# Kernel optimization log

Hardware: AMD Instinct MI355X
Metric: run time of the kernel (lower is better)

Reference implementation:

```python
import jax, jax.numpy as jnp
import numpy as np

H, C = 4, 64          # heads, per-head channels
NB, NG = 30000, 6000  # bus nodes, gen nodes
EL, EG = 250000, 12000

def setup_inputs():
    ks = iter(jax.random.split(jax.random.key(0), 64))
    def nrm(shape, scale=1.0):
        return jax.random.normal(next(ks), shape, jnp.float32) * scale
    inp = {}
    inp['x_bus'] = nrm((NB, 32))
    inp['x_gen'] = nrm((NG, 16))
    inp['ea_line'] = jax.random.uniform(next(ks), (EL, 6), jnp.float32)
    inp['ea_g2b'] = jax.random.uniform(next(ks), (EG, 6), jnp.float32)
    inp['ea_b2g'] = jax.random.uniform(next(ks), (EG, 6), jnp.float32)
    inp['proj_gen_w'] = nrm((16, 32), 16 ** -0.5)
    inp['proj_gen_b'] = jnp.zeros((32,), jnp.float32)
    for l, (din, dout) in enumerate([(32, 256), (256, 256), (256, 64)]):
        sc = din ** -0.5
        inp['Wl%d' % l] = nrm((3, din, H * C), sc)
        inp['Wr%d' % l] = nrm((3, din, H * C), sc)
        inp['We%d' % l] = nrm((3, 6, H * C), 6 ** -0.5)
        inp['att%d' % l] = nrm((3, H, C), 0.1)
        inp['bc%d' % l] = jnp.zeros((3, dout), jnp.float32)
        inp['temp%d' % l] = jnp.ones((3,), jnp.float32)
        inp['lnw%d' % l] = jnp.ones((2, dout), jnp.float32)
        inp['lnb%d' % l] = jnp.zeros((2, dout), jnp.float32)
    inp['rp0_w'] = nrm((2, 32, 256), 32 ** -0.5)
    inp['rp0_b'] = jnp.zeros((2, 256), jnp.float32)
    inp['rp2_w'] = nrm((2, 256, 64), 256 ** -0.5)
    inp['rp2_b'] = jnp.zeros((2, 64), jnp.float32)
    inp['src_line'] = jax.random.randint(next(ks), (EL,), 0, NB, jnp.int32)
    inp['dst_line'] = jax.random.randint(next(ks), (EL,), 0, NB, jnp.int32)
    inp['src_g2b'] = jax.random.randint(next(ks), (EG,), 0, NG, jnp.int32)
    inp['dst_g2b'] = jax.random.randint(next(ks), (EG,), 0, NB, jnp.int32)
    inp['src_b2g'] = jax.random.randint(next(ks), (EG,), 0, NB, jnp.int32)
    inp['dst_b2g'] = jax.random.randint(next(ks), (EG,), 0, NG, jnp.int32)
    return inp

def _conv(xs, xd, src, dst, ea, Wl, Wr, We, att, bias, temp, concat, nd):
    # PhysicsGATv2Conv: overwrite last edge-attr column with physics prior tau/|Z| (physics_weight=1, z_index=3)
    ea = ea.at[:, -1].set(temp / jnp.maximum(ea[:, 3], 1e-6))
    xl = (xs @ Wl).reshape(-1, H, C)   # [Ns,H,C]
    xr = (xd @ Wr).reshape(-1, H, C)   # [Nd,H,C]
    m = xl[src] + xr[dst] + (ea @ We).reshape(-1, H, C)  # [E,H,C]
    logits = (jax.nn.leaky_relu(m, 0.2) * att).sum(-1)   # [E,H]
    mx = jax.ops.segment_max(logits, dst, num_segments=nd)
    mx = jnp.where(jnp.isfinite(mx), mx, 0.0)
    ex = jnp.exp(logits - mx[dst])
    alpha = ex / (jax.ops.segment_sum(ex, dst, num_segments=nd)[dst] + 1e-16)
    o = jax.ops.segment_sum(xl[src] * alpha[..., None], dst, num_segments=nd)  # [Nd,H,C]
    o = o.reshape(nd, H * C) if concat else o.mean(1)
    return o + bias

def _ln(x, w, b):
    mu = x.mean(-1, keepdims=True)
    v = ((x - mu) ** 2).mean(-1, keepdims=True)
    return (x - mu) / jnp.sqrt(v + 1e-5) * w + b

def _fwd(x_bus, x_gen, ea_line, ea_g2b, ea_b2g, proj_gen_w, proj_gen_b,
         Wl0, Wr0, We0, att0, bc0, temp0, lnw0, lnb0,
         Wl1, Wr1, We1, att1, bc1, temp1, lnw1, lnb1,
         Wl2, Wr2, We2, att2, bc2, temp2, lnw2, lnb2,
         rp0_w, rp0_b, rp2_w, rp2_b,
         src_line, dst_line, src_g2b, dst_g2b, src_b2g, dst_b2g):
    xb = x_bus                               # bus projector is Identity (32 == max dim)
    xg = x_gen @ proj_gen_w + proj_gen_b     # gen 16 -> 32
    layers = [(Wl0, Wr0, We0, att0, bc0, temp0, lnw0, lnb0, True),
              (Wl1, Wr1, We1, att1, bc1, temp1, lnw1, lnb1, True),
              (Wl2, Wr2, We2, att2, bc2, temp2, lnw2, lnb2, False)]
    for l, (Wl, Wr, We, att, bc, tp, lw, lb, concat) in enumerate(layers):
        rb, rg = xb, xg
        # to_hetero aggr='sum': one conv per edge type, sum into destination node type
        ob = (_conv(xb, xb, src_line, dst_line, ea_line, Wl[0], Wr[0], We[0], att[0], bc[0], tp[0], concat, NB)
              + _conv(xg, xb, src_g2b, dst_g2b, ea_g2b, Wl[1], Wr[1], We[1], att[1], bc[1], tp[1], concat, NB))
        og = _conv(xb, xg, src_b2g, dst_b2g, ea_b2g, Wl[2], Wr[2], We[2], att[2], bc[2], tp[2], concat, NG)
        xb = _ln(ob, lw[0], lb[0])
        xg = _ln(og, lw[1], lb[1])
        if l == 0:
            xb = xb + rb @ rp0_w[0] + rp0_b[0]
            xg = xg + rg @ rp0_w[1] + rp0_b[1]
        elif l == 1:
            xb = xb + rb
            xg = xg + rg
        else:
            xb = xb + rb @ rp2_w[0] + rp2_b[0]
            xg = xg + rg @ rp2_w[1] + rp2_b[1]
        if l < 2:
            xb = jax.nn.elu(xb)
            xg = jax.nn.elu(xg)
    # output_projector is Identity (final_dim == output_dim == 64); concat node-type outputs
    return jnp.concatenate([xb, xg], 0)

def reference(x_bus, x_gen, ea_line, ea_g2b, ea_b2g, proj_gen_w, proj_gen_b,
              Wl0, Wr0, We0, att0, bc0, temp0, lnw0, lnb0,
              Wl1, Wr1, We1, att1, bc1, temp1, lnw1, lnb1,
              Wl2, Wr2, We2, att2, bc2, temp2, lnw2, lnb2,
              rp0_w, rp0_b, rp2_w, rp2_b,
              src_line, dst_line, src_g2b, dst_g2b, src_b2g, dst_b2g):
    return _fwd(x_bus, x_gen, ea_line, ea_g2b, ea_b2g, proj_gen_w, proj_gen_b,
                Wl0, Wr0, We0, att0, bc0, temp0, lnw0, lnb0,
                Wl1, Wr1, We1, att1, bc1, temp1, lnw1, lnb1,
                Wl2, Wr2, We2, att2, bc2, tem2 := temp2, lnw2, lnb2,
                rp0_w, rp0_b, rp2_w, rp2_b,
                src_line, dst_line, src_g2b, dst_g2b, src_b2g, dst_b2g)
```

## Files before the change

kernel.cpp:

```cpp
#include <hip/hip_runtime.h>
#include <math.h>

#define NBUS 30000
#define NGEN 6000
#define NEL 250000
#define NEG 12000

#define AS1 __attribute__((address_space(1)))
#define AS3 __attribute__((address_space(3)))

typedef unsigned short u16;
typedef __attribute__((ext_vector_type(8))) short bf16x8;
typedef __attribute__((ext_vector_type(4))) float f32x4;

__device__ __forceinline__ u16 f2b(float x) {
  unsigned u = __float_as_uint(x);
  unsigned r = (u + 0x7FFFu + ((u >> 16) & 1u)) >> 16;
  return (u16)r;
}
__device__ __forceinline__ float b2f(u16 x) {
  return __uint_as_float((unsigned)x << 16);
}
__device__ __forceinline__ f32x4 splat4(float v) {
  f32x4 r = {v, v, v, v};
  return r;
}
__device__ __forceinline__ f32x4 b2f4(ushort4 v) {
  f32x4 r;
  r.x = b2f(v.x); r.y = b2f(v.y); r.z = b2f(v.z); r.w = b2f(v.w);
  return r;
}

__global__ void zeroi(int* __restrict__ p, int n) {
  int i = blockIdx.x * blockDim.x + threadIdx.x;
  int st = gridDim.x * blockDim.x;
  for (; i < n; i += st) p[i] = 0;
}

__global__ void cast_k(const float* __restrict__ s, u16* __restrict__ d, int n) {
  int i = blockIdx.x * 256 + threadIdx.x;
  if (i < n) d[i] = f2b(s[i]);
}

struct CsrArgs {
  const int* dst[3];
  const int* src[3];
  const float* ea[3];
  const float* tmp0;
  const float* tmp1;
  const float* tmp2;
  int* cnt[3];
  int* rowptr[3];
  int* eidx[3];
  int* srcC[3];
  float* eaC[3];
  int* psum[3];
  int E[3];
  int N[3];
};

__global__ void hist_b(CsrArgs a) {
  int ty = blockIdx.y;
  int i = blockIdx.x * 256 + threadIdx.x;
  if (i < a.E[ty]) atomicAdd(&a.cnt[ty][a.dst[ty][i]], 1);
}

__global__ __launch_bounds__(1024) void scan_p1(CsrArgs a) {
  int ty = blockIdx.y;
  int n = a.N[ty];
  int base = blockIdx.x * 1024;
  if (base >= n) return;
  int tid = threadIdx.x, lane = tid & 63, wv = tid >> 6;
  int i = base + tid;
  int v = (i < n) ? a.cnt[ty][i] : 0;
#pragma unroll
  for (int off = 32; off >= 1; off >>= 1) v += __shfl_xor(v, off);
  __shared__ int w[16];
  if (lane == 0) w[wv] = v;
  __syncthreads();
  if (tid < 16) {
    int t = w[tid];
#pragma unroll
    for (int off = 8; off >= 1; off >>= 1) t += __shfl_xor(t, off, 16);
    if (tid == 0) a.psum[ty][blockIdx.x] = t;
  }
}

__global__ __launch_bounds__(64) void scan_p2(CsrArgs a) {
  int ty = blockIdx.y;
  int nb = (a.N[ty] + 1023) / 1024;
  int tid = threadIdx.x;
  int v = (tid < nb) ? a.psum[ty][tid] : 0;
  int x = v;
#pragma unroll
  for (int off = 1; off < 64; off <<= 1) {
    int y = __shfl_up(x, off, 64);
    if (tid >= off) x += y;
  }
  if (tid < nb) a.psum[ty][tid] = x - v;
}

__global__ __launch_bounds__(1024) void scan_p3(CsrArgs a) {
  int ty = blockIdx.y;
  int n = a.N[ty];
  int base = blockIdx.x * 1024;
  if (base >= n) return;
  int tid = threadIdx.x, lane = tid & 63, wv = tid >> 6;
  int i = base + tid;
  int v = (i < n) ? a.cnt[ty][i] : 0;
  int x = v;
#pragma unroll
  for (int off = 1; off < 64; off <<= 1) {
    int y = __shfl_up(x, off, 64);
    if (lane >= off) x += y;
  }
  __shared__ int w[16];
  if (lane == 63) w[wv] = x;
  __syncthreads();
  if (tid < 16) {
    int t = w[tid];
#pragma unroll
    for (int off = 1; off < 16; off <<= 1) {
      int y = __shfl_up(t, off, 16);
      if (tid >= off) t += y;
    }
    w[tid] = t;
  }
  __syncthreads();
  int woff = (wv == 0) ? 0 : w[wv - 1];
  int incl = a.psum[ty][blockIdx.x] + woff + x;
  if (i < n) {
    a.rowptr[ty][i + 1] = incl;
    a.cnt[ty][i] = incl - v;
  }
  if (i == 0) a.rowptr[ty][0] = 0;
}

__global__ void scatter_b(CsrArgs a) {
  int ty = blockIdx.y;
  int i = blockIdx.x * 256 + threadIdx.x;
  if (i < a.E[ty]) {
    int p = atomicAdd(&a.cnt[ty][a.dst[ty][i]], 1);
    a.eidx[ty][p] = i;
  }
}

__global__ void gather_b(CsrArgs a) {
  int ty = blockIdx.y;
  int i = blockIdx.x * 256 + threadIdx.x;
  if (i >= a.E[ty]) return;
  int e = a.eidx[ty][i];
  a.srcC[ty][i] = a.src[ty][e];
  const float* s = a.ea[ty] + (size_t)e * 6;
  float* d = a.eaC[ty] + (size_t)i * 8;
  float e3 = s[3];
  float inv = 1.f / fmaxf(e3, 1e-6f);
  d[0] = s[0]; d[1] = s[1]; d[2] = s[2]; d[3] = e3; d[4] = s[4];
  d[5] = a.tmp0[ty] * inv;
  d[6] = a.tmp1[ty] * inv;
  d[7] = a.tmp2[ty] * inv;
}

__global__ void gen_proj(const float* __restrict__ x, const float* __restrict__ w,
                         const float* __restrict__ b, u16* __restrict__ o16) {
  int idx = blockIdx.x * blockDim.x + threadIdx.x;
  if (idx >= NGEN * 32) return;
  int i = idx >> 5, c = idx & 31;
  float acc = b[c];
#pragma unroll
  for (int k = 0; k < 16; ++k) acc += x[i * 16 + k] * w[k * 32 + c];
  o16[idx] = f2b(acc);
}

struct PackArgs {
  const float* src[24];
  int off[24];
  int lgN[24];
  int total[24];
  int K[24];
};
__global__ void pack_multi(PackArgs a, u16* __restrict__ Wt) {
  int j = blockIdx.y;
  int idx = blockIdx.x * 256 + threadIdx.x;
  if (idx >= a.total[j]) return;
  int N1 = (1 << a.lgN[j]) - 1;
  int n = idx & N1;
  int k = idx >> a.lgN[j];
  Wt[(size_t)a.off[j] + (size_t)n * a.K[j] + k] = f2b(a.src[j][idx]);
}

__global__ __launch_bounds__(256) void gemm_both(
    const u16* __restrict__ Ab, const u16* __restrict__ Ag,
    const u16* __restrict__ Wt, int goff,
    u16* __restrict__ Cb, u16* __restrict__ Cg,
    int K, int Nb, int Ng, int ybus)
{
  __shared__ __align__(16) u16 As[128 * 32];
  __shared__ __align__(16) u16 Bs[128 * 32];
  const int t = threadIdx.x;
  const int w = t >> 6, lane = t & 63;
  const u16* A; const u16* W; u16* C; int M, Ncols, bn;
  if ((int)blockIdx.y < ybus) {
    A = Ab; W = Wt; C = Cb; M = NBUS; Ncols = Nb; bn = blockIdx.y * 128;
  } else {
    A = Ag; W = Wt + goff; C = Cg; M = NGEN; Ncols = Ng; bn = (blockIdx.y - ybus) * 128;
  }
  const int bm = blockIdx.x * 128;
  if (bm >= M) return;
  const int wm = (w & 1) * 64, wn = (w >> 1) * 64;
  const int lr = lane & 15, q = lane >> 4;
  const int srow = lane >> 2;
  const int blk = (lane & 3) ^ (srow & 3);
  f32x4 acc[4][4] = {};
  for (int k0 = 0; k0 < K; k0 += 32) {
#pragma unroll
    for (int sseg = 0; sseg < 2; ++sseg) {
      int seg = w + (sseg << 2);
      int row = (seg << 4) + srow;
      int ga = bm + row; if (ga > M - 1) ga = M - 1;
      const u16* gpa = A + (size_t)ga * K + k0 + (blk << 3);
      __builtin_amdgcn_global_load_lds((AS1 void*)gpa, (AS3 void*)(As + (seg << 9)),
                                       16, 0, 0);
      int gb = bn + row;
      const u16* gpb = W + (size_t)gb * K + k0 + (blk << 3);
      __builtin_amdgcn_global_load_lds((AS1 void*)gpb, (AS3 void*)(Bs + (seg << 9)),
                                       16, 0, 0);
    }
    __syncthreads();
    bf16x8 af[4], bg[4];
#pragma unroll
    for (int i = 0; i < 4; ++i) {
      int r = wm + i * 16 + lr;
      af[i] = *(const bf16x8*)&As[(r << 5) + ((q ^ (r & 3)) << 3)];
    }
#pragma unroll
    for (int j = 0; j < 4; ++j) {
      int r = wn + j * 16 + lr;
      bg[j] = *(const bf16x8*)&Bs[(r << 5) + ((q ^ (r & 3)) << 3)];
    }
#pragma unroll
    for (int i = 0; i < 4; ++i)
#pragma unroll
      for (int j = 0; j < 4; ++j)
        acc[i][j] = __builtin_amdgcn_mfma_f32_16x16x32_bf16(
            af[i], bg[j], acc[i][j], 0, 0, 0);
    __syncthreads();
  }
#pragma unroll
  for (int i = 0; i < 4; ++i) {
    int row0 = bm + wm + i * 16 + q * 4;
#pragma unroll
    for (int j = 0; j < 4; ++j) {
      int col = bn + wn + j * 16 + lr;
      if (col < Ncols) {
#pragma unroll
        for (int r = 0; r < 4; ++r) {
          int row = row0 + r;
          if (row < M) C[(size_t)row * Ncols + col] = f2b(acc[i][j][r]);
        }
      }
    }
  }
}


#define CS_F1(lv, ev, nv, tv, idx) do { \
    int rc_ = (idx) < nch ? (idx) : nch - 1; \
    lv = *(const ushort4*)(xl + (size_t)__builtin_amdgcn_readlane(vsrc, rc_) * ldl + ch); \
    const float* ep_ = eac + (size_t)(cb + rc_) * 8; \
    ev = *(const float4*)ep_; \
    nv = ep_[4]; \
    tv = ep_[4 + TS]; \
  } while (0)

#define CS_FETCH(S, base) do { \
    CS_F1(l##S##0, e##S##0, n##S##0, t##S##0, (base)); \
    CS_F1(l##S##1, e##S##1, n##S##1, t##S##1, (base) + 1); \
  } while (0)

#define CS_EDGE(xv, ev, nv, tv, pv) do { \
    f32x4 m_ = xv + rx; \
    m_ = __builtin_elementwise_fma(splat4(ev.x), w0, m_); \
    m_ = __builtin_elementwise_fma(splat4(ev.y), w1, m_); \
    m_ = __builtin_elementwise_fma(splat4(ev.z), w2, m_); \
    m_ = __builtin_elementwise_fma(splat4(ev.w), w3, m_); \
    m_ = __builtin_elementwise_fma(splat4(nv), w4, m_); \
    m_ = __builtin_elementwise_fma(splat4(tv), w5, m_); \
    m_ = __builtin_elementwise_max(m_, m_ * 0.2f); \
    pv = m_.x * av.x; \
    pv = fmaf(m_.y, av.y, pv); \
    pv = fmaf(m_.z, av.z, pv); \
    pv = fmaf(m_.w, av.w, pv); \
  } while (0)

#define CS_COMPUTE(S, base) do { \
    f32x4 x0_ = b2f4(l##S##0), x1_ = b2f4(l##S##1); \
    float p0_, p1_; \
    CS_EDGE(x0_, e##S##0, n##S##0, t##S##0, p0_); \
    CS_EDGE(x1_, e##S##1, n##S##1, t##S##1, p1_); \
    p0_ += __shfl_xor(p0_, 1); p0_ += __shfl_xor(p0_, 2); \
    p0_ += __shfl_xor(p0_, 4); p0_ += __shfl_xor(p0_, 8); \
    p1_ += __shfl_xor(p1_, 1); p1_ += __shfl_xor(p1_, 2); \
    p1_ += __shfl_xor(p1_, 4); p1_ += __shfl_xor(p1_, 8); \
    if ((base) >= nch) p0_ = -INFINITY; \
    if ((base) + 1 >= nch) p1_ = -INFINITY; \
    float nm_ = fmaxf(mx, fmaxf(p0_, p1_)); \
    float sc_ = __expf(mx - nm_); \
    float q0_ = __expf(p0_ - nm_), q1_ = __expf(p1_ - nm_); \
    mx = nm_; \
    den = den * sc_ + (q0_ + q1_); \
    acc = acc * splat4(sc_); \
    acc = __builtin_elementwise_fma(splat4(q0_), x0_, acc); \
    acc = __builtin_elementwise_fma(splat4(q1_), x1_, acc); \
  } while (0)

template<int TS>
__device__ __forceinline__ f32x4 conv_set(
    int node, int beg, int end, int ch,
    const int* __restrict__ srcc, const float* __restrict__ eac,
    const u16* __restrict__ xl, int ldl,
    const u16* __restrict__ xr, int ldr,
    const float* __restrict__ We, const float* __restrict__ att)
{
  f32x4 w0 = *(const f32x4*)(We + ch);
  f32x4 w1 = *(const f32x4*)(We + 256 + ch);
  f32x4 w2 = *(const f32x4*)(We + 512 + ch);
  f32x4 w3 = *(const f32x4*)(We + 768 + ch);
  f32x4 w4 = *(const f32x4*)(We + 1024 + ch);
  f32x4 w5 = *(const f32x4*)(We + 1280 + ch);
  f32x4 av = *(const f32x4*)(att + ch);
  f32x4 rx = b2f4(*(const ushort4*)(xr + (size_t)node * ldr + ch));
  float mx = -INFINITY, den = 0.f;
  f32x4 acc = {0.f, 0.f, 0.f, 0.f};
  int lane = ch >> 2;

  for (int cb = beg; cb < end; cb += 64) {
    int nch = end - cb;
    if (nch > 64) nch = 64;
    int li = lane < nch ? lane : nch - 1;
    int vsrc = srcc[cb + li];
    int np = (nch + 1) >> 1;

    ushort4 la0, la1, lb0, lb1;
    float4 ea0, ea1, eb0, eb1;
    float na0, na1, nb0, nb1;
    float ta0, ta1, tb0, tb1;

    CS_FETCH(a, 0);
    int g = 0;
    for (; g + 2 < np; g += 2) {
      CS_FETCH(b, (g + 1) << 1);
      CS_COMPUTE(a, g << 1);
      CS_FETCH(a, (g + 2) << 1);
      CS_COMPUTE(b, (g + 1) << 1);
    }
    if (g + 1 < np) {
      CS_FETCH(b, (g + 1) << 1);
      CS_COMPUTE(a, g << 1);
      CS_COMPUTE(b, (g + 1) << 1);
    } else {
      CS_COMPUTE(a, g << 1);
    }
  }
  float inv = 1.f / (den + 1e-16f);
  return acc * splat4(inv);
}

struct ConvP {
  const int* __restrict__ rpA; const int* __restrict__ srcA;
  const float* __restrict__ eaA;
  const u16* __restrict__ xlA; const u16* __restrict__ xrA;
  const float* __restrict__ WeA; const float* __restrict__ attA;
  const int* __restrict__ rpB; const int* __restrict__ srcB;
  const float* __restrict__ eaB;
  const u16* __restrict__ xlB; const u16* __restrict__ xrB;
  const float* __restrict__ WeB; const float* __restrict__ attB;
  const float* __restrict__ b1; const float* __restrict__ b2;
  const float* __restrict__ lnw; const float* __restrict__ lnb;
  const u16* __restrict__ res16;
  float* __restrict__ outf; u16* __restrict__ out16;
  int ldlA, ldrA, ldlB, ldrB, ld16, N;
};

template<int MODE, int TS>
__global__ __launch_bounds__(256) void conv_fused(ConvP bus, ConvP gen, int nbBus) {
  const bool isb = (int)blockIdx.x < nbBus;
  const int grp = isb ? blockIdx.x : blockIdx.x - nbBus;
#define SEL(f) (isb ? bus.f : gen.f)
  const int* __restrict__ rpA = SEL(rpA);
  const int* __restrict__ srcA = SEL(srcA);
  const float* __restrict__ eaA = SEL(eaA);
  const u16* __restrict__ xlA = SEL(xlA);
  const u16* __restrict__ xrA = SEL(xrA);
  const float* __restrict__ WeA = SEL(WeA);
  const float* __restrict__ attA = SEL(attA);
  const int* __restrict__ rpB = SEL(rpB);
  const int N = SEL(N);
  const int ldlA = SEL(ldlA), ldrA = SEL(ldrA);

  int node = grp * 4 + (threadIdx.x >> 6);
  int lane = threadIdx.x & 63;
  if (node >= N) return;
  int ch = lane << 2;
  int begA = rpA[node], endA = rpA[node + 1];
  int begB = 0, endB = 0;
  if (rpB) { begB = rpB[node]; endB = rpB[node + 1]; }
  f32x4 o = conv_set<TS>(node, begA, endA, ch, srcA, eaA, xlA, ldlA,
                         xrA, ldrA, WeA, attA);
  if (rpB && begB < endB) {
    f32x4 ob = conv_set<TS>(node, begB, endB, ch, SEL(srcB), SEL(eaB),
                            SEL(xlB), SEL(ldlB), SEL(xrB), SEL(ldrB),
                            SEL(WeB), SEL(attB));
    o[0] += ob[0]; o[1] += ob[1]; o[2] += ob[2]; o[3] += ob[3];
  }
  const float* __restrict__ b1 = SEL(b1);
  const float* __restrict__ b2 = SEL(b2);
  const float* __restrict__ lnw = SEL(lnw);
  const float* __restrict__ lnb = SEL(lnb);
  const u16* __restrict__ res16 = SEL(res16);
  const int ld16 = SEL(ld16);
  if (MODE == 0) {
    int c = ch;
    float4 bb = *(const float4*)(b1 + c);
    float v0 = o[0] + bb.x, v1 = o[1] + bb.y, v2 = o[2] + bb.z, v3 = o[3] + bb.w;
    if (b2) {
      float4 b2v = *(const float4*)(b2 + c);
      v0 += b2v.x; v1 += b2v.y; v2 += b2v.z; v3 += b2v.w;
    }
    float s = v0 + v1 + v2 + v3;
#pragma unroll
    for (int m = 32; m >= 1; m >>= 1) s += __shfl_xor(s, m);
    float mu = s * (1.f / 256.f);
    float d0 = v0 - mu, d1 = v1 - mu, d2 = v2 - mu, d3 = v3 - mu;
    float q = d0*d0 + d1*d1 + d2*d2 + d3*d3;
#pragma unroll
    for (int m = 32; m >= 1; m >>= 1) q += __shfl_xor(q, m);
    float rs = rsqrtf(q * (1.f / 256.f) + 1e-5f);
    float4 lw = *(const float4*)(lnw + c);
    float4 lb = *(const float4*)(lnb + c);
    float y0 = d0 * rs * lw.x + lb.x;
    float y1 = d1 * rs * lw.y + lb.y;
    float y2 = d2 * rs * lw.z + lb.z;
    float y3 = d3 * rs * lw.w + lb.w;
    ushort4 r = *(const ushort4*)(res16 + (size_t)node * ld16 + c);
    y0 += b2f(r.x); y1 += b2f(r.y); y2 += b2f(r.z); y3 += b2f(r.w);
    y0 = (y0 > 0.f) ? y0 : expm1f(y0);
    y1 = (y1 > 0.f) ? y1 : expm1f(y1);
    y2 = (y2 > 0.f) ? y2 : expm1f(y2);
    y3 = (y3 > 0.f) ? y3 : expm1f(y3);
    ushort4 o16;
    o16.x = f2b(y0); o16.y = f2b(y1); o16.z = f2b(y2); o16.w = f2b(y3);
    u16* __restrict__ out16 = SEL(out16);
    *(ushort4*)(out16 + (size_t)node * 256 + c) = o16;
  } else {
    float h0 = o[0], h1 = o[1], h2 = o[2], h3 = o[3];
    h0 += __shfl_xor(h0, 16); h0 += __shfl_xor(h0, 32);
    h1 += __shfl_xor(h1, 16); h1 += __shfl_xor(h1, 32);
    h2 += __shfl_xor(h2, 16); h2 += __shfl_xor(h2, 32);
    h3 += __shfl_xor(h3, 16); h3 += __shfl_xor(h3, 32);
    int cc = (lane & 15) << 2;
    float4 bb = *(const float4*)(b1 + cc);
    float v0 = 0.25f * h0 + bb.x, v1 = 0.25f * h1 + bb.y;
    float v2 = 0.25f * h2 + bb.z, v3 = 0.25f * h3 + bb.w;
    if (b2) {
      float4 b2v = *(const float4*)(b2 + cc);
      v0 += b2v.x; v1 += b2v.y; v2 += b2v.z; v3 += b2v.w;
    }
    float s = v0 + v1 + v2 + v3;
#pragma unroll
    for (int m = 8; m >= 1; m >>= 1) s += __shfl_xor(s, m);
    float mu = s * (1.f / 64.f);
    float d0 = v0 - mu, d1 = v1 - mu, d2 = v2 - mu, d3 = v3 - mu;
    float q = d0*d0 + d1*d1 + d2*d2 + d3*d3;
#pragma unroll
    for (int m = 8; m >= 1; m >>= 1) q += __shfl_xor(q, m);
    float rs = rsqrtf(q * (1.f / 64.f) + 1e-5f);
    float4 lw = *(const float4*)(lnw + cc);
    float4 lb = *(const float4*)(lnb + cc);
    ushort4 r = *(const ushort4*)(res16 + (size_t)node * ld16 + cc);
    float y0 = d0 * rs * lw.x + lb.x + b2f(r.x);
    float y1 = d1 * rs * lw.y + lb.y + b2f(r.y);
    float y2 = d2 * rs * lw.z + lb.z + b2f(r.z);
    float y3 = d3 * rs * lw.w + lb.w + b2f(r.w);
    float* __restrict__ outf = SEL(outf);
    if (lane < 16)
      *(float4*)(outf + (size_t)node * 64 + cc) = make_float4(y0, y1, y2, y3);
  }
#undef SEL
}

extern "C" void kernel_launch(void* const* d_in, const int* in_sizes, int n_in,
                              void* d_out, int out_size, void* d_ws, size_t ws_size,
                              hipStream_t stream) {
  const float* x_bus = (const float*)d_in[0];
  const float* x_gen = (const float*)d_in[1];
  const float* ea[3] = {(const float*)d_in[2], (const float*)d_in[3], (const float*)d_in[4]};
  const float* pw = (const float*)d_in[5];
  const float* pb = (const float*)d_in[6];
  const float* Wl[3] = {(const float*)d_in[7], (const float*)d_in[15], (const float*)d_in[23]};
  const float* Wr[3] = {(const float*)d_in[8], (const float*)d_in[16], (const float*)d_in[24]};
  const float* We[3] = {(const float*)d_in[9], (const float*)d_in[17], (const float*)d_in[25]};
  const float* att[3] = {(const float*)d_in[10], (const float*)d_in[18], (const float*)d_in[26]};
  const float* bc[3] = {(const float*)d_in[11], (const float*)d_in[19], (const float*)d_in[27]};
  const float* temp[3] = {(const float*)d_in[12], (const float*)d_in[20], (const float*)d_in[28]};
  const float* lnw[3] = {(const float*)d_in[13], (const float*)d_in[21], (const float*)d_in[29]};
  const float* lnb[3] = {(const float*)d_in[14], (const float*)d_in[22], (const float*)d_in[30]};
  const float* rp0_w = (const float*)d_in[31];
  const float* rp2_w = (const float*)d_in[33];
  const int* srcs[3] = {(const int*)d_in[35], (const int*)d_in[37], (const int*)d_in[39]};
  const int* dsts[3] = {(const int*)d_in[36], (const int*)d_in[38], (const int*)d_in[40]};

  float* ws = (float*)d_ws;
  size_t off = 0;
  auto alloc = [&](size_t n) { float* p = ws + off; off += n; return p; };
  u16* xb16_0 = (u16*)alloc((size_t)NBUS * 16);
  u16* xg16_0 = (u16*)alloc((size_t)NGEN * 16);
  u16* xb16 = (u16*)alloc((size_t)NBUS * 128);
  u16* xg16 = (u16*)alloc((size_t)NGEN * 128);
  u16* Pbus = (u16*)alloc((size_t)NBUS * 640);
  u16* Pgen = (u16*)alloc((size_t)NGEN * 384);
  u16* Wt = (u16*)alloc((size_t)886000 / 2);
  float* eaC0 = alloc((size_t)NEL * 8);
  float* eaC1 = alloc((size_t)NEG * 8);
  float* eaC2 = alloc((size_t)NEG * 8);
  int* cw_all = (int*)alloc(NBUS + NBUS + NGEN);
  int* rp_line = (int*)alloc(NBUS + 1);
  int* rp_g2b = (int*)alloc(NBUS + 1);
  int* rp_b2g = (int*)alloc(NGEN + 1);
  int* ei_line = (int*)alloc(NEL);
  int* ei_g2b = (int*)alloc(NEG);
  int* ei_b2g = (int*)alloc(NEG);
  int* sc_line = (int*)alloc(NEL);
  int* sc_g2b = (int*)alloc(NEG);
  int* sc_b2g = (int*)alloc(NEG);
  int* psum = (int*)alloc(3 * 32);
  (void)ws_size; (void)in_sizes; (void)n_in; (void)out_size;

  CsrArgs ca;
  for (int t = 0; t < 3; ++t) { ca.dst[t] = dsts[t]; ca.src[t] = srcs[t]; ca.ea[t] = ea[t]; }
  ca.tmp0 = temp[0]; ca.tmp1 = temp[1]; ca.tmp2 = temp[2];
  ca.cnt[0] = cw_all; ca.cnt[1] = cw_all + NBUS; ca.cnt[2] = cw_all + 2 * NBUS;
  ca.rowptr[0] = rp_line; ca.rowptr[1] = rp_g2b; ca.rowptr[2] = rp_b2g;
  ca.eidx[0] = ei_line; ca.eidx[1] = ei_g2b; ca.eidx[2] = ei_b2g;
  ca.srcC[0] = sc_line; ca.srcC[1] = sc_g2b; ca.srcC[2] = sc_b2g;
  ca.eaC[0] = eaC0; ca.eaC[1] = eaC1; ca.eaC[2] = eaC2;
  ca.psum[0] = psum; ca.psum[1] = psum + 32; ca.psum[2] = psum + 64;
  ca.E[0] = NEL; ca.E[1] = NEG; ca.E[2] = NEG;
  ca.N[0] = NBUS; ca.N[1] = NBUS; ca.N[2] = NGEN;

  int egrid = (NEL + 255) / 256;
  hipLaunchKernelGGL(zeroi, dim3(64), dim3(1024), 0, stream, cw_all, 2 * NBUS + NGEN);
  hipLaunchKernelGGL(hist_b, dim3(egrid, 3), dim3(256), 0, stream, ca);
  hipLaunchKernelGGL(scan_p1, dim3(30, 3), dim3(1024), 0, stream, ca);
  hipLaunchKernelGGL(scan_p2, dim3(1, 3), dim3(64), 0, stream, ca);
  hipLaunchKernelGGL(scan_p3, dim3(30, 3), dim3(1024), 0, stream, ca);
  hipLaunchKernelGGL(scatter_b, dim3(egrid, 3), dim3(256), 0, stream, ca);
  hipLaunchKernelGGL(gather_b, dim3(egrid, 3), dim3(256), 0, stream, ca);

  hipLaunchKernelGGL(gen_proj, dim3((NGEN * 32 + 255) / 256), dim3(256), 0, stream,
                     x_gen, pw, pb, xg16_0);
  hipLaunchKernelGGL(cast_k, dim3((NBUS * 32 + 255) / 256), dim3(256), 0, stream,
                     x_bus, xb16_0, NBUS * 32);

  const int K_l[3] = {32, 256, 256};
  const int Nbus_l[3] = {1280, 1024, 1088};
  const int Ngen_l[3] = {768, 512, 576};
  int Lbase[3], goff_l[3];
  {
    int b = 0;
    for (int l = 0; l < 3; ++l) {
      Lbase[l] = b;
      goff_l[l] = Nbus_l[l] * K_l[l];
      b += (Nbus_l[l] + Ngen_l[l]) * K_l[l];
    }
  }
  PackArgs pa = {};
  int ns = 0;
  auto add = [&](const float* src, int offel, int N_, int lg, int K) {
    pa.src[ns] = src; pa.off[ns] = offel; pa.lgN[ns] = lg;
    pa.total[ns] = K * N_; pa.K[ns] = K; ++ns;
  };
  for (int l = 0; l < 3; ++l) {
    int K = K_l[l];
    size_t sl = (size_t)K * 256;
    int L = Lbase[l], go = goff_l[l];
    add(Wl[l], L, 256, 8, K);
    add(Wr[l], L + 256 * K, 256, 8, K);
    add(Wr[l] + sl, L + 512 * K, 256, 8, K);
    add(Wl[l] + 2 * sl, L + 768 * K, 256, 8, K);
    add(Wl[l] + sl, L + go, 256, 8, K);
    add(Wr[l] + 2 * sl, L + go + 256 * K, 256, 8, K);
    if (l == 0) {
      add(rp0_w, L + 1024 * K, 256, 8, K);
      add(rp0_w + 32 * 256, L + go + 512 * K, 256, 8, K);
    } else if (l == 2) {
      add(rp2_w, L + 1024 * K, 64, 6, K);
      add(rp2_w + 256 * 64, L + go + 512 * K, 64, 6, K);
    }
  }
  hipLaunchKernelGGL(pack_multi, dim3(256, ns), dim3(256), 0, stream, pa, Wt);

  const int nbBus = (NBUS + 3) / 4;
  const int nbGen = (NGEN + 3) / 4;

  for (int l = 0; l < 3; ++l) {
    const int K = K_l[l];
    const int Nb = Nbus_l[l], Ng = Ngen_l[l];
    const u16* Ab = (l == 0) ? xb16_0 : xb16;
    const u16* Ag = (l == 0) ? xg16_0 : xg16;

    int ybus = (Nb + 127) / 128, ygen = (Ng + 127) / 128;
    hipLaunchKernelGGL(gemm_both, dim3((NBUS + 127) / 128, ybus + ygen),
                       dim3(256), 0, stream,
                       Ab, Ag, Wt + Lbase[l], goff_l[l], Pbus, Pgen, K, Nb, Ng, ybus);

    ConvP pb_ = {};
    pb_.rpA = rp_line; pb_.srcA = sc_line; pb_.eaA = eaC0;
    pb_.xlA = Pbus; pb_.ldlA = Nb; pb_.xrA = Pbus + 256; pb_.ldrA = Nb;
    pb_.WeA = We[l]; pb_.attA = att[l];
    pb_.rpB = rp_g2b; pb_.srcB = sc_g2b; pb_.eaB = eaC1;
    pb_.xlB = Pgen; pb_.ldlB = Ng; pb_.xrB = Pbus + 512; pb_.ldrB = Nb;
    pb_.WeB = We[l] + 1536; pb_.attB = att[l] + 256;
    pb_.N = NBUS;
    ConvP pg_ = {};
    pg_.rpA = rp_b2g; pg_.srcA = sc_b2g; pg_.eaA = eaC2;
    pg_.xlA = Pbus + 768; pg_.ldlA = Nb; pg_.xrA = Pgen + 256; pg_.ldrA = Ng;
    pg_.WeA = We[l] + 3072; pg_.attA = att[l] + 512;
    pg_.rpB = nullptr;
    pg_.N = NGEN;
    dim3 gall(nbBus + nbGen), blk(256);

    if (l < 2) {
      pb_.b1 = bc[l]; pb_.b2 = bc[l] + 256; pb_.lnw = lnw[l]; pb_.lnb = lnb[l];
      pg_.b1 = bc[l] + 512; pg_.b2 = nullptr;
      pg_.lnw = lnw[l] + 256; pg_.lnb = lnb[l] + 256;
      if (l == 0) {
        pb_.res16 = Pbus + 1024; pb_.ld16 = Nb;
        pg_.res16 = Pgen + 512; pg_.ld16 = Ng;
      } else {
        pb_.res16 = xb16; pb_.ld16 = 256;
        pg_.res16 = xg16; pg_.ld16 = 256;
      }
      pb_.outf = nullptr; pb_.out16 = xb16;
      pg_.outf = nullptr; pg_.out16 = xg16;
      if (l == 0)
        hipLaunchKernelGGL((conv_fused<0, 1>), gall, blk, 0, stream, pb_, pg_, nbBus);
      else
        hipLaunchKernelGGL((conv_fused<0, 2>), gall, blk, 0, stream, pb_, pg_, nbBus);
    } else {
      pb_.b1 = bc[2]; pb_.b2 = bc[2] + 64; pb_.lnw = lnw[2]; pb_.lnb = lnb[2];
      pb_.res16 = Pbus + 1024; pb_.ld16 = Nb;
      pb_.outf = (float*)d_out; pb_.out16 = nullptr;
      pg_.b1 = bc[2] + 128; pg_.b2 = nullptr; pg_.lnw = lnw[2] + 64; pg_.lnb = lnb[2] + 64;
      pg_.res16 = Pgen + 512; pg_.ld16 = Ng;
      pg_.outf = (float*)d_out + (size_t)NBUS * 64; pg_.out16 = nullptr;
      hipLaunchKernelGGL((conv_fused<1, 3>), gall, blk, 0, stream, pb_, pg_, nbBus);
    }
  }
}
```

Measured before the change: 532.7 us.

## Use persistent conv blocks with atomic per-wave node work stealing

The fused GAT conv kernel becomes persistent: a fixed grid of blocks (1888 bus + 160 gen) loops, and each wave grabs the next destination node through an atomic counter instead of mapping one node per wave statically. The goal is to even out load imbalance from skewed node in-degrees and to cut block launch overhead. The counters live in the zeroed workspace, one pair per layer. The cost is one global atomic per node and possible contention, plus a fixed grid sized by hand.

```diff
diff --git a/kernel.cpp b/kernel.cpp
--- a/kernel.cpp
+++ b/kernel.cpp
@@ -383,9 +383,12 @@
 };
 
 template<int MODE, int TS>
-__global__ __launch_bounds__(256) void conv_fused(ConvP bus, ConvP gen, int nbBus) {
+__global__ __launch_bounds__(256) void conv_fused(
+    ConvP bus, ConvP gen, int nbBus,
+    int* __restrict__ cntB, int* __restrict__ cntG)
+{
   const bool isb = (int)blockIdx.x < nbBus;
-  const int grp = isb ? blockIdx.x : blockIdx.x - nbBus;
+  int* __restrict__ cnt = isb ? cntB : cntG;
 #define SEL(f) (isb ? bus.f : gen.f)
   const int* __restrict__ rpA = SEL(rpA);
   const int* __restrict__ srcA = SEL(srcA);
@@ -397,94 +400,100 @@
   const int* __restrict__ rpB = SEL(rpB);
   const int N = SEL(N);
   const int ldlA = SEL(ldlA), ldrA = SEL(ldrA);
-
-  int node = grp * 4 + (threadIdx.x >> 6);
-  int lane = threadIdx.x & 63;
-  if (node >= N) return;
-  int ch = lane << 2;
-  int begA = rpA[node], endA = rpA[node + 1];
-  int begB = 0, endB = 0;
-  if (rpB) { begB = rpB[node]; endB = rpB[node + 1]; }
-  f32x4 o = conv_set<TS>(node, begA, endA, ch, srcA, eaA, xlA, ldlA,
-                         xrA, ldrA, WeA, attA);
-  if (rpB && begB < endB) {
-    f32x4 ob = conv_set<TS>(node, begB, endB, ch, SEL(srcB), SEL(eaB),
-                            SEL(xlB), SEL(ldlB), SEL(xrB), SEL(ldrB),
-                            SEL(WeB), SEL(attB));
-    o[0] += ob[0]; o[1] += ob[1]; o[2] += ob[2]; o[3] += ob[3];
-  }
   const float* __restrict__ b1 = SEL(b1);
   const float* __restrict__ b2 = SEL(b2);
   const float* __restrict__ lnw = SEL(lnw);
   const float* __restrict__ lnb = SEL(lnb);
   const u16* __restrict__ res16 = SEL(res16);
   const int ld16 = SEL(ld16);
-  if (MODE == 0) {
-    int c = ch;
-    float4 bb = *(const float4*)(b1 + c);
-    float v0 = o[0] + bb.x, v1 = o[1] + bb.y, v2 = o[2] + bb.z, v3 = o[3] + bb.w;
-    if (b2) {
-      float4 b2v = *(const float4*)(b2 + c);
-      v0 += b2v.x; v1 += b2v.y; v2 += b2v.z; v3 += b2v.w;
-    }
-    float s = v0 + v1 + v2 + v3;
-#pragma unroll
-    for (int m = 32; m >= 1; m >>= 1) s += __shfl_xor(s, m);
-    float mu = s * (1.f / 256.f);
-    float d0 = v0 - mu, d1 = v1 - mu, d2 = v2 - mu, d3 = v3 - mu;
-    float q = d0*d0 + d1*d1 + d2*d2 + d3*d3;
-#pragma unroll
-    for (int m = 32; m >= 1; m >>= 1) q += __shfl_xor(q, m);
-    float rs = rsqrtf(q * (1.f / 256.f) + 1e-5f);
-    float4 lw = *(const float4*)(lnw + c);
-    float4 lb = *(const float4*)(lnb + c);
-    float y0 = d0 * rs * lw.x + lb.x;
-    float y1 = d1 * rs * lw.y + lb.y;
-    float y2 = d2 * rs * lw.z + lb.z;
-    float y3 = d3 * rs * lw.w + lb.w;
-    ushort4 r = *(const ushort4*)(res16 + (size_t)node * ld16 + c);
-    y0 += b2f(r.x); y1 += b2f(r.y); y2 += b2f(r.z); y3 += b2f(r.w);
-    y0 = (y0 > 0.f) ? y0 : expm1f(y0);
-    y1 = (y1 > 0.f) ? y1 : expm1f(y1);
-    y2 = (y2 > 0.f) ? y2 : expm1f(y2);
-    y3 = (y3 > 0.f) ? y3 : expm1f(y3);
-    ushort4 o16;
-    o16.x = f2b(y0); o16.y = f2b(y1); o16.z = f2b(y2); o16.w = f2b(y3);
-    u16* __restrict__ out16 = SEL(out16);
-    *(ushort4*)(out16 + (size_t)node * 256 + c) = o16;
-  } else {
-    float h0 = o[0], h1 = o[1], h2 = o[2], h3 = o[3];
-    h0 += __shfl_xor(h0, 16); h0 += __shfl_xor(h0, 32);
-    h1 += __shfl_xor(h1, 16); h1 += __shfl_xor(h1, 32);
-    h2 += __shfl_xor(h2, 16); h2 += __shfl_xor(h2, 32);
-    h3 += __shfl_xor(h3, 16); h3 += __shfl_xor(h3, 32);
-    int cc = (lane & 15) << 2;
-    float4 bb = *(const float4*)(b1 + cc);
-    float v0 = 0.25f * h0 + bb.x, v1 = 0.25f * h1 + bb.y;
-    float v2 = 0.25f * h2 + bb.z, v3 = 0.25f * h3 + bb.w;
-    if (b2) {
-      float4 b2v = *(const float4*)(b2 + cc);
-      v0 += b2v.x; v1 += b2v.y; v2 += b2v.z; v3 += b2v.w;
-    }
-    float s = v0 + v1 + v2 + v3;
-#pragma unroll
-    for (int m = 8; m >= 1; m >>= 1) s += __shfl_xor(s, m);
-    float mu = s * (1.f / 64.f);
-    float d0 = v0 - mu, d1 = v1 - mu, d2 = v2 - mu, d3 = v3 - mu;
-    float q = d0*d0 + d1*d1 + d2*d2 + d3*d3;
-#pragma unroll
-    for (int m = 8; m >= 1; m >>= 1) q += __shfl_xor(q, m);
-    float rs = rsqrtf(q * (1.f / 64.f) + 1e-5f);
-    float4 lw = *(const float4*)(lnw + cc);
-    float4 lb = *(const float4*)(lnb + cc);
-    ushort4 r = *(const ushort4*)(res16 + (size_t)node * ld16 + cc);
-    float y0 = d0 * rs * lw.x + lb.x + b2f(r.x);
-    float y1 = d1 * rs * lw.y + lb.y + b2f(r.y);
-    float y2 = d2 * rs * lw.z + lb.z + b2f(r.z);
-    float y3 = d3 * rs * lw.w + lb.w + b2f(r.w);
-    float* __restrict__ outf = SEL(outf);
-    if (lane < 16)
-      *(float4*)(outf + (size_t)node * 64 + cc) = make_float4(y0, y1, y2, y3);
+
+  const int lane = threadIdx.x & 63;
+  const int ch = lane << 2;
+
+  for (;;) {
+    int n0 = 0;
+    if (lane == 0) n0 = atomicAdd(cnt, 1);
+    const int node = __builtin_amdgcn_readfirstlane(n0);
+    if (node >= N) break;
+
+    int begA = rpA[node], endA = rpA[node + 1];
+    int begB = 0, endB = 0;
+    if (rpB) { begB = rpB[node]; endB = rpB[node + 1]; }
+    f32x4 o = conv_set<TS>(node, begA, endA, ch, srcA, eaA, xlA, ldlA,
+                           xrA, ldrA, WeA, attA);
+    if (rpB && begB < endB) {
+      f32x4 ob = conv_set<TS>(node, begB, endB, ch, SEL(srcB), SEL(eaB),
+                              SEL(xlB), SEL(ldlB), SEL(xrB), SEL(ldrB),
+                              SEL(WeB), SEL(attB));
+      o[0] += ob[0]; o[1] += ob[1]; o[2] += ob[2]; o[3] += ob[3];
+    }
+    if (MODE == 0) {
+      int c = ch;
+      float4 bb = *(const float4*)(b1 + c);
+      float v0 = o[0] + bb.x, v1 = o[1] + bb.y, v2 = o[2] + bb.z, v3 = o[3] + bb.w;
+      if (b2) {
+        float4 b2v = *(const float4*)(b2 + c);
+        v0 += b2v.x; v1 += b2v.y; v2 += b2v.z; v3 += b2v.w;
+      }
+      float s = v0 + v1 + v2 + v3;
+#pragma unroll
+      for (int m = 32; m >= 1; m >>= 1) s += __shfl_xor(s, m);
+      float mu = s * (1.f / 256.f);
+      float d0 = v0 - mu, d1 = v1 - mu, d2 = v2 - mu, d3 = v3 - mu;
+      float q = d0*d0 + d1*d1 + d2*d2 + d3*d3;
+#pragma unroll
+      for (int m = 32; m >= 1; m >>= 1) q += __shfl_xor(q, m);
+      float rs = rsqrtf(q * (1.f / 256.f) + 1e-5f);
+      float4 lw = *(const float4*)(lnw + c);
+      float4 lb = *(const float4*)(lnb + c);
+      float y0 = d0 * rs * lw.x + lb.x;
+      float y1 = d1 * rs * lw.y + lb.y;
+      float y2 = d2 * rs * lw.z + lb.z;
+      float y3 = d3 * rs * lw.w + lb.w;
+      ushort4 r = *(const ushort4*)(res16 + (size_t)node * ld16 + c);
+      y0 += b2f(r.x); y1 += b2f(r.y); y2 += b2f(r.z); y3 += b2f(r.w);
+      y0 = (y0 > 0.f) ? y0 : expm1f(y0);
+      y1 = (y1 > 0.f) ? y1 : expm1f(y1);
+      y2 = (y2 > 0.f) ? y2 : expm1f(y2);
+      y3 = (y3 > 0.f) ? y3 : expm1f(y3);
+      ushort4 o16;
+      o16.x = f2b(y0); o16.y = f2b(y1); o16.z = f2b(y2); o16.w = f2b(y3);
+      u16* __restrict__ out16 = SEL(out16);
+      *(ushort4*)(out16 + (size_t)node * 256 + c) = o16;
+    } else {
+      float h0 = o[0], h1 = o[1], h2 = o[2], h3 = o[3];
+      h0 += __shfl_xor(h0, 16); h0 += __shfl_xor(h0, 32);
+      h1 += __shfl_xor(h1, 16); h1 += __shfl_xor(h1, 32);
+      h2 += __shfl_xor(h2, 16); h2 += __shfl_xor(h2, 32);
+      h3 += __shfl_xor(h3, 16); h3 += __shfl_xor(h3, 32);
+      int cc = (lane & 15) << 2;
+      float4 bb = *(const float4*)(b1 + cc);
+      float v0 = 0.25f * h0 + bb.x, v1 = 0.25f * h1 + bb.y;
+      float v2 = 0.25f * h2 + bb.z, v3 = 0.25f * h3 + bb.w;
+      if (b2) {
+        float4 b2v = *(const float4*)(b2 + cc);
+        v0 += b2v.x; v1 += b2v.y; v2 += b2v.z; v3 += b2v.w;
+      }
+      float s = v0 + v1 + v2 + v3;
+#pragma unroll
+      for (int m = 8; m >= 1; m >>= 1) s += __shfl_xor(s, m);
+      float mu = s * (1.f / 64.f);
+      float d0 = v0 - mu, d1 = v1 - mu, d2 = v2 - mu, d3 = v3 - mu;
+      float q = d0*d0 + d1*d1 + d2*d2 + d3*d3;
+#pragma unroll
+      for (int m = 8; m >= 1; m >>= 1) q += __shfl_xor(q, m);
+      float rs = rsqrtf(q * (1.f / 64.f) + 1e-5f);
+      float4 lw = *(const float4*)(lnw + cc);
+      float4 lb = *(const float4*)(lnb + cc);
+      ushort4 r = *(const ushort4*)(res16 + (size_t)node * ld16 + cc);
+      float y0 = d0 * rs * lw.x + lb.x + b2f(r.x);
+      float y1 = d1 * rs * lw.y + lb.y + b2f(r.y);
+      float y2 = d2 * rs * lw.z + lb.z + b2f(r.z);
+      float y3 = d3 * rs * lw.w + lb.w + b2f(r.w);
+      float* __restrict__ outf = SEL(outf);
+      if (lane < 16)
+        *(float4*)(outf + (size_t)node * 64 + cc) = make_float4(y0, y1, y2, y3);
+    }
   }
 #undef SEL
 }
@@ -523,7 +532,8 @@
   float* eaC0 = alloc((size_t)NEL * 8);
   float* eaC1 = alloc((size_t)NEG * 8);
   float* eaC2 = alloc((size_t)NEG * 8);
-  int* cw_all = (int*)alloc(NBUS + NBUS + NGEN);
+  int* cw_all = (int*)alloc(NBUS + NBUS + NGEN + 8);
+  int* nodecnt = cw_all + 2 * NBUS + NGEN;
   int* rp_line = (int*)alloc(NBUS + 1);
   int* rp_g2b = (int*)alloc(NBUS + 1);
   int* rp_b2g = (int*)alloc(NGEN + 1);
@@ -549,7 +559,7 @@
   ca.N[0] = NBUS; ca.N[1] = NBUS; ca.N[2] = NGEN;
 
   int egrid = (NEL + 255) / 256;
-  hipLaunchKernelGGL(zeroi, dim3(64), dim3(1024), 0, stream, cw_all, 2 * NBUS + NGEN);
+  hipLaunchKernelGGL(zeroi, dim3(64), dim3(1024), 0, stream, cw_all, 2 * NBUS + NGEN + 8);
   hipLaunchKernelGGL(hist_b, dim3(egrid, 3), dim3(256), 0, stream, ca);
   hipLaunchKernelGGL(scan_p1, dim3(30, 3), dim3(1024), 0, stream, ca);
   hipLaunchKernelGGL(scan_p2, dim3(1, 3), dim3(64), 0, stream, ca);
@@ -600,8 +610,8 @@
   }
   hipLaunchKernelGGL(pack_multi, dim3(256, ns), dim3(256), 0, stream, pa, Wt);
 
-  const int nbBus = (NBUS + 3) / 4;
-  const int nbGen = (NGEN + 3) / 4;
+  const int nbBus = 1888;
+  const int nbGen = 160;
 
   for (int l = 0; l < 3; ++l) {
     const int K = K_l[l];
@@ -629,6 +639,8 @@
     pg_.rpB = nullptr;
     pg_.N = NGEN;
     dim3 gall(nbBus + nbGen), blk(256);
+    int* cB = nodecnt + 2 * l;
+    int* cG = nodecnt + 2 * l + 1;
 
     if (l < 2) {
       pb_.b1 = bc[l]; pb_.b2 = bc[l] + 256; pb_.lnw = lnw[l]; pb_.lnb = lnb[l];
@@ -644,9 +656,9 @@
       pb_.outf = nullptr; pb_.out16 = xb16;
       pg_.outf = nullptr; pg_.out16 = xg16;
       if (l == 0)
-        hipLaunchKernelGGL((conv_fused<0, 1>), gall, blk, 0, stream, pb_, pg_, nbBus);
+        hipLaunchKernelGGL((conv_fused<0, 1>), gall, blk, 0, stream, pb_, pg_, nbBus, cB, cG);
       else
-        hipLaunchKernelGGL((conv_fused<0, 2>), gall, blk, 0, stream, pb_, pg_, nbBus);
+        hipLaunchKernelGGL((conv_fused<0, 2>), gall, blk, 0, stream, pb_, pg_, nbBus, cB, cG);
     } else {
       pb_.b1 = bc[2]; pb_.b2 = bc[2] + 64; pb_.lnw = lnw[2]; pb_.lnb = lnb[2];
       pb_.res16 = Pbus + 1024; pb_.ld16 = Nb;
@@ -654,7 +666,7 @@
       pg_.b1 = bc[2] + 128; pg_.b2 = nullptr; pg_.lnw = lnw[2] + 64; pg_.lnb = lnb[2] + 64;
       pg_.res16 = Pgen + 512; pg_.ld16 = Ng;
       pg_.outf = (float*)d_out + (size_t)NBUS * 64; pg_.out16 = nullptr;
-      hipLaunchKernelGGL((conv_fused<1, 3>), gall, blk, 0, stream, pb_, pg_, nbBus);
-    }
-  }
-}
+      hipLaunchKernelGGL((conv_fused<1, 3>), gall, blk, 0, stream, pb_, pg_, nbBus, cB, cG);
+    }
+  }
+}
```

Result: slower. 1.851 ms (+247.4%).
